# Optimization experiments

Measured on AMD Instinct MI355X. Metric: run time of the kernel, lower is better.

The kernel has to match this reference:

```python
import jax, jax.numpy as jnp
import numpy as np

NIBBLE_SHIFTS = jnp.arange(8, dtype=jnp.int32) * 4


def _unpack_int4(packed):
    # packed: [..., P] int32 -> [..., P*8] int32 values in [0, 15]
    vals = (packed[..., None] >> NIBBLE_SHIFTS) & 0xF
    return vals.reshape(*packed.shape[:-1], packed.shape[-1] * 8)


def setup_inputs() -> dict:
    key = jax.random.key(0)
    k1, k2, k3, k4, k5, k6 = jax.random.split(key, 6)
    M, K, N, G = 4096, 4096, 11008, 128
    inp = jax.random.normal(k1, (M, K), dtype=jnp.float32)
    qweight = jax.random.randint(k2, (K, N // 8), 0, 2147483647, dtype=jnp.int32)
    woq_scales = jax.random.uniform(k3, (K // G, N), dtype=jnp.float32)
    woq_qzeros = jax.random.randint(k4, (K // G, N // 8), 0, 2147483647, dtype=jnp.int32)
    woq_bias = jax.random.normal(k5, (N,), dtype=jnp.float32)
    mul = jax.random.normal(k6, (M, N), dtype=jnp.float32)
    return {"inp": inp, "qweight": qweight, "woq_scales": woq_scales,
            "woq_qzeros": woq_qzeros, "woq_bias": woq_bias, "mul": mul,
            "group_size": G}


def reference(inp, qweight, woq_scales, woq_qzeros, woq_bias, mul, group_size):
    K = qweight.shape[0]
    # dequantize int4 weights: w = (q - z) * scale, per group of `group_size` K-rows
    w_int = _unpack_int4(qweight).astype(jnp.float32)            # [K, N]
    z_int = _unpack_int4(woq_qzeros).astype(jnp.float32)         # [K/G, N]
    zeros_full = jnp.repeat(z_int, group_size, axis=0)           # [K, N]
    scales_full = jnp.repeat(woq_scales, group_size, axis=0)     # [K, N]
    w = (w_int - zeros_full) * scales_full                       # [K, N]
    woq_out = inp @ w + woq_bias                                 # [M, N]
    return jax.nn.silu(woq_out) * mul
```

## Files before the change

kernel.cpp:

```cpp
#include <hip/hip_runtime.h>
#include <hip/hip_bf16.h>

typedef __attribute__((ext_vector_type(8))) short short8;
typedef __attribute__((ext_vector_type(4))) short short4v;
typedef __attribute__((ext_vector_type(4))) float float4v;

__device__ __forceinline__ short f2bf(float f) {
  union { float f; unsigned u; } v; v.f = f;
  unsigned r = v.u + 0x7fffu + ((v.u >> 16) & 1u);
  return (short)(r >> 16);
}

typedef const __attribute__((address_space(1))) unsigned int* as1_u32p;
typedef __attribute__((address_space(3))) unsigned int* as3_u32p;

__device__ __forceinline__ void gl_lds16(const void* g, void* l) {
  __builtin_amdgcn_global_load_lds((as1_u32p)g, (as3_u32p)l, 16, 0, 0);
}

__global__ __launch_bounds__(256, 4)
void dequant_kernel(const int* __restrict__ qw,
                    const float* __restrict__ scales,
                    const int* __restrict__ qzeros,
                    short* __restrict__ Bt,
                    int K, int N, int G)
{
  constexpr int KP = 72;
  __shared__ short Ls[256 * KP];
  const int N8  = N >> 3;
  const int k0  = blockIdx.x * 64;
  const int n0  = blockIdx.y * 256;
  const int n80 = blockIdx.y * 32;
  const int g   = k0 / G;
  const int t   = threadIdx.x;
  const int kloc = t >> 3;
  const int w4   = (t & 7) * 4;

  const int4 z4 = *(const int4*)(qzeros + (size_t)g * N8 + n80 + w4);
  const int za[4] = {z4.x, z4.y, z4.z, z4.w};
  float sc[32];
  #pragma unroll
  for (int ii = 0; ii < 8; ++ii)
    *(float4v*)(sc + ii * 4) =
        *(const float4v*)(scales + (size_t)g * N + n0 + w4 * 8 + ii * 4);

  #pragma unroll
  for (int kh = 0; kh < 2; ++kh) {
    const int k = kloc + kh * 32;
    const int4 q4 = *(const int4*)(qw + (size_t)(k0 + k) * N8 + n80 + w4);
    const int qa[4] = {q4.x, q4.y, q4.z, q4.w};
    #pragma unroll
    for (int ii = 0; ii < 4; ++ii) {
      #pragma unroll
      for (int j = 0; j < 8; ++j) {
        const float z = (float)((za[ii] >> (4 * j)) & 0xF);
        const float q = (float)((qa[ii] >> (4 * j)) & 0xF);
        Ls[(w4 * 8 + ii * 8 + j) * KP + k] = f2bf((q - z) * sc[ii * 8 + j]);
      }
    }
  }
  __syncthreads();

  #pragma unroll
  for (int it = 0; it < 8; ++it) {
    const int idx = t + it * 256;
    const int row = idx >> 3;
    const int ch  = (idx & 7) * 8;
    const short8 v = *(const short8*)(&Ls[row * KP + ch]);
    *(short8*)(Bt + (size_t)(n0 + row) * K + k0 + ch) = v;
  }
}

__global__ __launch_bounds__(256, 2)
void dequant_kernel_v0(const int* __restrict__ qw,
                       const float* __restrict__ scales,
                       const int* __restrict__ qzeros,
                       short* __restrict__ Bt,
                       int K, int N, int G)
{
  __shared__ short Ls[128 * 64];
  const int N8  = N >> 3;
  const int k0  = blockIdx.x * 64;
  const int n80 = blockIdx.y * 16;
  const int g   = k0 / G;
  const int tid  = threadIdx.x;
  const int lane = tid & 63;
  const int w    = tid >> 6;

  const int4 q4 = *(const int4*)(qw + (size_t)(k0 + lane) * N8 + n80 + w * 4);
  const int4 z4 = *(const int4*)(qzeros + (size_t)g * N8 + n80 + w * 4);
  const int qa[4] = {q4.x, q4.y, q4.z, q4.w};
  const int za[4] = {z4.x, z4.y, z4.z, z4.w};

  #pragma unroll
  for (int it = 0; it < 4; ++it) {
    const int n8l = w * 4 + it;
    const float4v s0 = *(const float4v*)(scales + (size_t)g * N + (n80 + n8l) * 8);
    const float4v s1 = *(const float4v*)(scales + (size_t)g * N + (n80 + n8l) * 8 + 4);
    const float sc[8] = {s0[0], s0[1], s0[2], s0[3], s1[0], s1[1], s1[2], s1[3]};
    const int wq = qa[it], wz = za[it];
    #pragma unroll
    for (int j = 0; j < 8; ++j) {
      const float z = (float)((wz >> (4 * j)) & 0xF);
      const float q = (float)((wq >> (4 * j)) & 0xF);
      Ls[(n8l * 8 + j) * 64 + lane] = f2bf((q - z) * sc[j]);
    }
  }
  __syncthreads();

  #pragma unroll
  for (int it = 0; it < 4; ++it) {
    const int c   = tid + it * 256;
    const int row = c >> 3;
    const int off = (c & 7) * 8;
    const short8 v = *(const short8*)(&Ls[row * 64 + off]);
    *(short8*)(Bt + (size_t)(n80 * 8 + row) * K + k0 + off) = v;
  }
}

__global__ __launch_bounds__(256, 4)
void aconv_kernel(const float* __restrict__ in, short* __restrict__ out, long long n)
{
  const long long i = ((long long)blockIdx.x * blockDim.x + threadIdx.x) * 8;
  if (i >= n) return;
  const float4v a = *(const float4v*)(in + i);
  const float4v b = *(const float4v*)(in + i + 4);
  short8 h;
  h[0] = f2bf(a[0]); h[1] = f2bf(a[1]); h[2] = f2bf(a[2]); h[3] = f2bf(a[3]);
  h[4] = f2bf(b[0]); h[5] = f2bf(b[1]); h[6] = f2bf(b[2]); h[7] = f2bf(b[3]);
  *(short8*)(out + i) = h;
}

__global__ __launch_bounds__(512, 2)
void gemm256_silu_mul_kernel(const short* __restrict__ A,
                             const short* __restrict__ Bt,
                             const float* __restrict__ bias,
                             const float* __restrict__ mulp,
                             float*       __restrict__ out,
                             int M, int N, int K)
{
  __shared__ short L[2][2][16384];

  const int tid  = threadIdx.x;
  const int lane = tid & 63;
  const int wave = tid >> 6;
  const int wm   = wave >> 2;
  const int wn   = wave & 3;

  const int nwg = gridDim.x;
  const int q8 = nwg >> 3, r8 = nwg & 7;
  const int xcd = blockIdx.x & 7, sub = blockIdx.x >> 3;
  const int swz = (xcd < r8 ? xcd * (q8 + 1) : r8 * (q8 + 1) + (xcd - r8) * q8) + sub;
  const int nbx = N >> 8;
  const int bx = swz % nbx, by = swz / nbx;
  const int m0 = by << 8, n0 = bx << 8;

  const short* Ab = A  + (size_t)m0 * K;
  const short* Bb = Bt + (size_t)n0 * K;

  const int srow = lane >> 2;
  const int scol = (((lane & 3) ^ ((lane & 32) >> 4))) * 8;
  const int fm = lane & 15;
  const int ko = ((lane >> 4) * 8) ^ ((fm & 8) ? 16 : 0);

  const int BG0 = wave * 2;
  const int BG1 = wave * 2 + 1;
  const int AEg = (wave & 3) + (wave >> 2) * 8;
  const int ALg = AEg + 4;

  float4v acc[8][4];
  #pragma unroll
  for (int i = 0; i < 8; ++i)
    #pragma unroll
    for (int j = 0; j < 4; ++j)
      acc[i][j] = (float4v){0.f, 0.f, 0.f, 0.f};

  const int NT = K >> 6;

  auto stage2 = [&](int buf, int ab, int g, const short* __restrict__ base, int kk) {
    #pragma unroll
    for (int ks = 0; ks < 2; ++ks)
      gl_lds16(base + (size_t)(g * 16 + srow) * K + kk + ks * 32 + scol,
               &L[buf][ab][(g * 2 + ks) * 512]);
  };

  stage2(0, 0, AEg, Ab, 0);
  stage2(0, 1, BG0, Bb, 0);
  stage2(0, 1, BG1, Bb, 0);
  stage2(0, 0, ALg, Ab, 0);
  asm volatile("s_waitcnt vmcnt(4)" ::: "memory");
  __builtin_amdgcn_s_barrier();

  for (int t = 0; t < NT; ++t) {
    const int cur = t & 1;
    const int nxt = cur ^ 1;
    const int kk1 = (t + 1) << 6;
    const bool pf = (t + 1) < NT;

    short8 af[4][2], bf[4][2];

    #pragma unroll
    for (int i = 0; i < 4; ++i)
      #pragma unroll
      for (int ks = 0; ks < 2; ++ks)
        af[i][ks] = *(const short8*)(
            &L[cur][0][((wm * 8 + i) * 2 + ks) * 512 + fm * 32 + ko]);
    #pragma unroll
    for (int j = 0; j < 4; j += 2)
      #pragma unroll
      for (int ks = 0; ks < 2; ++ks)
        bf[j][ks] = *(const short8*)(
            &L[cur][1][((wn * 4 + j) * 2 + ks) * 512 + fm * 32 + ko]);
    if (pf) stage2(nxt, 0, AEg, Ab, kk1);
    __builtin_amdgcn_s_barrier();
    asm volatile("s_waitcnt lgkmcnt(0)" ::: "memory");
    __builtin_amdgcn_sched_barrier(0);
    __builtin_amdgcn_s_setprio(1);
    #pragma unroll
    for (int i = 0; i < 4; ++i)
      #pragma unroll
      for (int j = 0; j < 4; j += 2)
        #pragma unroll
        for (int ks = 0; ks < 2; ++ks)
          acc[i][j] = __builtin_amdgcn_mfma_f32_16x16x32_bf16(
              af[i][ks], bf[j][ks], acc[i][j], 0, 0, 0);
    __builtin_amdgcn_s_setprio(0);
    if (pf) { asm volatile("s_waitcnt vmcnt(4)" ::: "memory"); }
    else    { asm volatile("s_waitcnt vmcnt(2)" ::: "memory"); }
    __builtin_amdgcn_s_barrier();

    #pragma unroll
    for (int j = 1; j < 4; j += 2)
      #pragma unroll
      for (int ks = 0; ks < 2; ++ks)
        bf[j][ks] = *(const short8*)(
            &L[cur][1][((wn * 4 + j) * 2 + ks) * 512 + fm * 32 + ko]);
    if (pf) stage2(nxt, 1, BG0, Bb, kk1);
    __builtin_amdgcn_s_barrier();
    asm volatile("s_waitcnt lgkmcnt(0)" ::: "memory");
    __builtin_amdgcn_sched_barrier(0);
    __builtin_amdgcn_s_setprio(1);
    #pragma unroll
    for (int i = 0; i < 4; ++i)
      #pragma unroll
      for (int j = 1; j < 4; j += 2)
        #pragma unroll
        for (int ks = 0; ks < 2; ++ks)
          acc[i][j] = __builtin_amdgcn_mfma_f32_16x16x32_bf16(
              af[i][ks], bf[j][ks], acc[i][j], 0, 0, 0);
    __builtin_amdgcn_s_setprio(0);
    if (pf) { asm volatile("s_waitcnt vmcnt(4)" ::: "memory"); }
    else    { asm volatile("s_waitcnt vmcnt(0)" ::: "memory"); }
    __builtin_amdgcn_s_barrier();

    #pragma unroll
    for (int i = 0; i < 4; ++i)
      #pragma unroll
      for (int ks = 0; ks < 2; ++ks)
        af[i][ks] = *(const short8*)(
            &L[cur][0][((wm * 8 + 4 + i) * 2 + ks) * 512 + fm * 32 + ko]);
    if (pf) stage2(nxt, 1, BG1, Bb, kk1);
    __builtin_amdgcn_s_barrier();
    asm volatile("s_waitcnt lgkmcnt(0)" ::: "memory");
    __builtin_amdgcn_sched_barrier(0);
    __builtin_amdgcn_s_setprio(1);
    #pragma unroll
    for (int i = 0; i < 4; ++i)
      #pragma unroll
      for (int j = 0; j < 4; j += 2)
        #pragma unroll
        for (int ks = 0; ks < 2; ++ks)
          acc[4 + i][j] = __builtin_amdgcn_mfma_f32_16x16x32_bf16(
              af[i][ks], bf[j][ks], acc[4 + i][j], 0, 0, 0);
    __builtin_amdgcn_s_setprio(0);
    __builtin_amdgcn_s_barrier();

    if (pf) stage2(nxt, 0, ALg, Ab, kk1);
    __builtin_amdgcn_s_barrier();
    __builtin_amdgcn_s_setprio(1);
    #pragma unroll
    for (int i = 0; i < 4; ++i)
      #pragma unroll
      for (int j = 1; j < 4; j += 2)
        #pragma unroll
        for (int ks = 0; ks < 2; ++ks)
          acc[4 + i][j] = __builtin_amdgcn_mfma_f32_16x16x32_bf16(
              af[i][ks], bf[j][ks], acc[4 + i][j], 0, 0, 0);
    __builtin_amdgcn_s_setprio(0);
    if (pf) { asm volatile("s_waitcnt vmcnt(4)" ::: "memory"); }
    __builtin_amdgcn_s_barrier();
  }

  const int cn  = lane & 15;
  const int cr4 = (lane >> 4) * 4;
  #pragma unroll
  for (int mt = 0; mt < 8; ++mt) {
    #pragma unroll
    for (int nt = 0; nt < 4; ++nt) {
      const int n  = n0 + wn * 64 + nt * 16 + cn;
      const float bn = bias[n];
      #pragma unroll
      for (int i = 0; i < 4; ++i) {
        const int m = m0 + wm * 128 + mt * 16 + cr4 + i;
        float x = acc[mt][nt][i] + bn;
        float s = x / (1.0f + __expf(-x));
        out[(size_t)m * N + n] = s * mulp[(size_t)m * N + n];
      }
    }
  }
}

__global__ __launch_bounds__(256, 2)
void gemm_silu_mul_kernel(const short* __restrict__ A,
                          const short* __restrict__ Bt,
                          const float* __restrict__ bias,
                          const float* __restrict__ mulp,
                          float*       __restrict__ out,
                          int M, int N, int K)
{
  __shared__ short As[128 * 64];
  __shared__ short Bs[128 * 64];

  const int tid  = threadIdx.x;
  const int lane = tid & 63;
  const int wave = tid >> 6;
  const int wr = (wave >> 1) * 64;
  const int wc = (wave & 1) * 64;
  const int m0 = blockIdx.y * 128;
  const int n0 = blockIdx.x * 128;

  float4v acc[4][4];
  #pragma unroll
  for (int i = 0; i < 4; ++i)
    #pragma unroll
    for (int j = 0; j < 4; ++j)
      acc[i][j] = (float4v){0.f, 0.f, 0.f, 0.f};

  const int fm = lane & 15;
  const int fk = (lane >> 4) * 8;
  const int srow = lane >> 3;
  const int scol = (lane & 7) * 8;

  for (int k0 = 0; k0 < K; k0 += 64) {
    #pragma unroll
    for (int c = 0; c < 4; ++c) {
      const int chunk = wave * 4 + c;
      const int row   = chunk * 8 + srow;
      gl_lds16(A  + (size_t)(m0 + row) * K + k0 + scol, &As[chunk * 512]);
      gl_lds16(Bt + (size_t)(n0 + row) * K + k0 + scol, &Bs[chunk * 512]);
    }
    __syncthreads();

    #pragma unroll
    for (int ks = 0; ks < 64; ks += 32) {
      short8 a[4], b[4];
      #pragma unroll
      for (int mt = 0; mt < 4; ++mt)
        a[mt] = *(const short8*)(&As[(wr + mt * 16 + fm) * 64 + ks + fk]);
      #pragma unroll
      for (int nt = 0; nt < 4; ++nt)
        b[nt] = *(const short8*)(&Bs[(wc + nt * 16 + fm) * 64 + ks + fk]);
      #pragma unroll
      for (int mt = 0; mt < 4; ++mt)
        #pragma unroll
        for (int nt = 0; nt < 4; ++nt)
          acc[mt][nt] = __builtin_amdgcn_mfma_f32_16x16x32_bf16(a[mt], b[nt], acc[mt][nt], 0, 0, 0);
    }
    __syncthreads();
  }

  const int cn = lane & 15;
  const int cr = (lane >> 4) * 4;
  #pragma unroll
  for (int mt = 0; mt < 4; ++mt) {
    #pragma unroll
    for (int nt = 0; nt < 4; ++nt) {
      const int n  = n0 + wc + nt * 16 + cn;
      const float bn = bias[n];
      #pragma unroll
      for (int i = 0; i < 4; ++i) {
        const int m = m0 + wr + mt * 16 + cr + i;
        float x = acc[mt][nt][i] + bn;
        float s = x / (1.0f + __expf(-x));
        out[(size_t)m * N + n] = s * mulp[(size_t)m * N + n];
      }
    }
  }
}

#define BM 128
#define BN 128
#define BK 64
#define LDA 72
#define LDB 72

__global__ __launch_bounds__(256, 2)
void woq_silu_mul_kernel(const float* __restrict__ inp, const int* __restrict__ qw,
                         const float* __restrict__ scales, const int* __restrict__ qzeros,
                         const float* __restrict__ bias, const float* __restrict__ mulp,
                         float* __restrict__ out, int M, int N, int K, int G)
{
  __shared__ short As[BM * LDA];
  __shared__ short Bs[BN * LDB];
  const int tid  = threadIdx.x;
  const int lane = tid & 63;
  const int wave = tid >> 6;
  const int wr = (wave >> 1) * 64;
  const int wc = (wave & 1) * 64;
  const int m0 = blockIdx.y * BM;
  const int n0 = blockIdx.x * BN;
  const int N8 = N >> 3;
  float4v acc[4][4];
  #pragma unroll
  for (int i = 0; i < 4; ++i)
    #pragma unroll
    for (int j = 0; j < 4; ++j)
      acc[i][j] = (float4v){0.f, 0.f, 0.f, 0.f};
  const int n8l  = tid >> 4;
  const int kloc = (tid & 15) * 4;
  const int fm = lane & 15;
  const int fk = (lane >> 4) * 8;
  for (int k0 = 0; k0 < K; k0 += BK) {
    #pragma unroll
    for (int i = 0; i < 8; ++i) {
      int f = tid + i * 256;
      int row = f >> 4;
      int col = (f & 15) * 4;
      float4v a4 = *(const float4v*)(inp + (size_t)(m0 + row) * K + k0 + col);
      short4v h;
      h[0] = f2bf(a4[0]); h[1] = f2bf(a4[1]); h[2] = f2bf(a4[2]); h[3] = f2bf(a4[3]);
      *(short4v*)(&As[row * LDA + col]) = h;
    }
    {
      const int g = k0 / G;
      const int n8g = (n0 >> 3) + n8l;
      const int zw = qzeros[(size_t)g * N8 + n8g];
      const float4v s0 = *(const float4v*)(scales + (size_t)g * N + n0 + n8l * 8);
      const float4v s1 = *(const float4v*)(scales + (size_t)g * N + n0 + n8l * 8 + 4);
      float sc[8] = {s0[0], s0[1], s0[2], s0[3], s1[0], s1[1], s1[2], s1[3]};
      int w[4];
      #pragma unroll
      for (int kk = 0; kk < 4; ++kk)
        w[kk] = qw[(size_t)(k0 + kloc + kk) * N8 + n8g];
      #pragma unroll
      for (int j = 0; j < 8; ++j) {
        const float zj = (float)((zw >> (4 * j)) & 0xF);
        const float sj = sc[j];
        short4v h;
        #pragma unroll
        for (int kk = 0; kk < 4; ++kk) {
          int q = (w[kk] >> (4 * j)) & 0xF;
          h[kk] = f2bf(((float)q - zj) * sj);
        }
        *(short4v*)(&Bs[(n8l * 8 + j) * LDB + kloc]) = h;
      }
    }
    __syncthreads();
    #pragma unroll
    for (int ks = 0; ks < BK; ks += 32) {
      short8 a[4], b[4];
      #pragma unroll
      for (int mt = 0; mt < 4; ++mt)
        a[mt] = *(const short8*)(&As[(wr + mt * 16 + fm) * LDA + ks + fk]);
      #pragma unroll
      for (int nt = 0; nt < 4; ++nt)
        b[nt] = *(const short8*)(&Bs[(wc + nt * 16 + fm) * LDB + ks + fk]);
      #pragma unroll
      for (int mt = 0; mt < 4; ++mt)
        #pragma unroll
        for (int nt = 0; nt < 4; ++nt)
          acc[mt][nt] = __builtin_amdgcn_mfma_f32_16x16x32_bf16(a[mt], b[nt], acc[mt][nt], 0, 0, 0);
    }
    __syncthreads();
  }
  const int cn = lane & 15;
  const int cr = (lane >> 4) * 4;
  #pragma unroll
  for (int mt = 0; mt < 4; ++mt) {
    #pragma unroll
    for (int nt = 0; nt < 4; ++nt) {
      const int n = n0 + wc + nt * 16 + cn;
      const float bn = bias[n];
      #pragma unroll
      for (int i = 0; i < 4; ++i) {
        const int m = m0 + wr + mt * 16 + cr + i;
        float x = acc[mt][nt][i] + bn;
        float s = x / (1.0f + __expf(-x));
        out[(size_t)m * N + n] = s * mulp[(size_t)m * N + n];
      }
    }
  }
}

extern "C" void kernel_launch(void* const* d_in, const int* in_sizes, int n_in,
                              void* d_out, int out_size, void* d_ws, size_t ws_size,
                              hipStream_t stream) {
  const float* inp    = (const float*)d_in[0];
  const int*   qw     = (const int*)d_in[1];
  const float* scales = (const float*)d_in[2];
  const int*   qzeros = (const int*)d_in[3];
  const float* bias   = (const float*)d_in[4];
  const float* mulp   = (const float*)d_in[5];
  float*       out    = (float*)d_out;

  const int N = in_sizes[4];
  const int K = (int)(((long long)in_sizes[1] * 8) / N);
  const int M = (int)((long long)in_sizes[0] / K);
  const int G = K / (in_sizes[2] / N);

  const size_t btBytes = (size_t)N * K * sizeof(short);
  const size_t aBytes  = (size_t)M * K * sizeof(short);

  if (ws_size >= btBytes + aBytes) {
    short* Bt  = (short*)d_ws;
    short* Abf = (short*)((char*)d_ws + btBytes);

    if ((N & 255) == 0 && (K & 63) == 0 && (64 % (K / (in_sizes[2] / N) > 64 ? 64 : 1)) == 0) {
      dim3 dq_grid(K / 64, N / 256);
      dequant_kernel<<<dq_grid, dim3(256), 0, stream>>>(qw, scales, qzeros, Bt, K, N, G);
    } else {
      dim3 dq_grid(K / 64, (N / 8) / 16);
      dequant_kernel_v0<<<dq_grid, dim3(256), 0, stream>>>(qw, scales, qzeros, Bt, K, N, G);
    }

    const long long nA = (long long)M * K;
    aconv_kernel<<<dim3((unsigned)((nA / 8 + 255) / 256)), dim3(256), 0, stream>>>(inp, Abf, nA);

    if ((M & 255) == 0 && (N & 255) == 0 && (K & 63) == 0) {
      dim3 grid((unsigned)((N >> 8) * (M >> 8)));
      gemm256_silu_mul_kernel<<<grid, dim3(512), 0, stream>>>(Abf, Bt, bias, mulp, out, M, N, K);
    } else {
      dim3 grid(N / 128, M / 128);
      gemm_silu_mul_kernel<<<grid, dim3(256), 0, stream>>>(Abf, Bt, bias, mulp, out, M, N, K);
    }
  } else {
    dim3 grid(N / BN, M / BM);
    woq_silu_mul_kernel<<<grid, dim3(256), 0, stream>>>(inp, qw, scales, qzeros,
                                                        bias, mulp, out, M, N, K, G);
  }
}
```

Measured before the change: 707.5 us.

## Fuse dequant and A-conversion launches; deepen GEMM prefetch to two stages ahead

The weight dequantization and the fp32-to-bf16 activation conversion now run in one launch, with the block index choosing which role a block takes, so one kernel launch and its tail are removed. Separately, the GEMM main loop now issues global-to-LDS loads two k-tiles ahead instead of one, with new vmcnt wait counts, so more memory latency can overlap MFMA work. The deeper prefetch relies on hand-tuned waitcnt values and on a reordered staging sequence that writes into the buffer currently being read. That raises the risk of LDS races and adds more outstanding loads per wave.

```diff
diff --git a/kernel.cpp b/kernel.cpp
--- a/kernel.cpp
+++ b/kernel.cpp
@@ -19,18 +19,36 @@
 }
 
 __global__ __launch_bounds__(256, 4)
-void dequant_kernel(const int* __restrict__ qw,
-                    const float* __restrict__ scales,
-                    const int* __restrict__ qzeros,
-                    short* __restrict__ Bt,
-                    int K, int N, int G)
+void prep_kernel(const int* __restrict__ qw,
+                 const float* __restrict__ scales,
+                 const int* __restrict__ qzeros,
+                 short* __restrict__ Bt,
+                 const float* __restrict__ inp,
+                 short* __restrict__ Abf,
+                 int K, int N, int G, int nDq, long long nA)
 {
   constexpr int KP = 72;
   __shared__ short Ls[256 * KP];
+
+  if ((int)blockIdx.x >= nDq) {
+    const long long i =
+        (((long long)blockIdx.x - nDq) * blockDim.x + threadIdx.x) * 8;
+    if (i >= nA) return;
+    const float4v a = *(const float4v*)(inp + i);
+    const float4v b = *(const float4v*)(inp + i + 4);
+    short8 h;
+    h[0] = f2bf(a[0]); h[1] = f2bf(a[1]); h[2] = f2bf(a[2]); h[3] = f2bf(a[3]);
+    h[4] = f2bf(b[0]); h[5] = f2bf(b[1]); h[6] = f2bf(b[2]); h[7] = f2bf(b[3]);
+    *(short8*)(Abf + i) = h;
+    return;
+  }
+
+  const int KB  = K >> 6;
   const int N8  = N >> 3;
-  const int k0  = blockIdx.x * 64;
-  const int n0  = blockIdx.y * 256;
-  const int n80 = blockIdx.y * 32;
+  const int k0  = ((int)blockIdx.x % KB) * 64;
+  const int nb  = (int)blockIdx.x / KB;
+  const int n0  = nb * 256;
+  const int n80 = nb * 32;
   const int g   = k0 / G;
   const int t   = threadIdx.x;
   const int kloc = t >> 3;
@@ -188,14 +206,23 @@
   stage2(0, 1, BG0, Bb, 0);
   stage2(0, 1, BG1, Bb, 0);
   stage2(0, 0, ALg, Ab, 0);
-  asm volatile("s_waitcnt vmcnt(4)" ::: "memory");
+  if (NT > 1) {
+    stage2(1, 0, AEg, Ab, 64);
+    stage2(1, 1, BG0, Bb, 64);
+    stage2(1, 1, BG1, Bb, 64);
+    asm volatile("s_waitcnt vmcnt(10)" ::: "memory");
+  } else {
+    asm volatile("s_waitcnt vmcnt(4)" ::: "memory");
+  }
   __builtin_amdgcn_s_barrier();
 
   for (int t = 0; t < NT; ++t) {
     const int cur = t & 1;
     const int nxt = cur ^ 1;
+    const bool i1 = (t + 1) < NT;
+    const bool i2 = (t + 2) < NT;
     const int kk1 = (t + 1) << 6;
-    const bool pf = (t + 1) < NT;
+    const int kk2 = (t + 2) << 6;
 
     short8 af[4][2], bf[4][2];
 
@@ -211,7 +238,7 @@
       for (int ks = 0; ks < 2; ++ks)
         bf[j][ks] = *(const short8*)(
             &L[cur][1][((wn * 4 + j) * 2 + ks) * 512 + fm * 32 + ko]);
-    if (pf) stage2(nxt, 0, AEg, Ab, kk1);
+    if (i1) stage2(nxt, 0, ALg, Ab, kk1);
     __builtin_amdgcn_s_barrier();
     asm volatile("s_waitcnt lgkmcnt(0)" ::: "memory");
     __builtin_amdgcn_sched_barrier(0);
@@ -225,8 +252,8 @@
           acc[i][j] = __builtin_amdgcn_mfma_f32_16x16x32_bf16(
               af[i][ks], bf[j][ks], acc[i][j], 0, 0, 0);
     __builtin_amdgcn_s_setprio(0);
-    if (pf) { asm volatile("s_waitcnt vmcnt(4)" ::: "memory"); }
-    else    { asm volatile("s_waitcnt vmcnt(2)" ::: "memory"); }
+    if (i1) { asm volatile("s_waitcnt vmcnt(10)" ::: "memory"); }
+    else    { asm volatile("s_waitcnt vmcnt(2)"  ::: "memory"); }
     __builtin_amdgcn_s_barrier();
 
     #pragma unroll
@@ -235,7 +262,7 @@
       for (int ks = 0; ks < 2; ++ks)
         bf[j][ks] = *(const short8*)(
             &L[cur][1][((wn * 4 + j) * 2 + ks) * 512 + fm * 32 + ko]);
-    if (pf) stage2(nxt, 1, BG0, Bb, kk1);
+    if (i2) stage2(cur, 0, AEg, Ab, kk2);
     __builtin_amdgcn_s_barrier();
     asm volatile("s_waitcnt lgkmcnt(0)" ::: "memory");
     __builtin_amdgcn_sched_barrier(0);
@@ -249,8 +276,9 @@
           acc[i][j] = __builtin_amdgcn_mfma_f32_16x16x32_bf16(
               af[i][ks], bf[j][ks], acc[i][j], 0, 0, 0);
     __builtin_amdgcn_s_setprio(0);
-    if (pf) { asm volatile("s_waitcnt vmcnt(4)" ::: "memory"); }
-    else    { asm volatile("s_waitcnt vmcnt(0)" ::: "memory"); }
+    if (i2)      { asm volatile("s_waitcnt vmcnt(10)" ::: "memory"); }
+    else if (i1) { asm volatile("s_waitcnt vmcnt(8)"  ::: "memory"); }
+    else         { asm volatile("s_waitcnt vmcnt(0)"  ::: "memory"); }
     __builtin_amdgcn_s_barrier();
 
     #pragma unroll
@@ -259,7 +287,7 @@
       for (int ks = 0; ks < 2; ++ks)
         af[i][ks] = *(const short8*)(
             &L[cur][0][((wm * 8 + 4 + i) * 2 + ks) * 512 + fm * 32 + ko]);
-    if (pf) stage2(nxt, 1, BG1, Bb, kk1);
+    if (i2) stage2(cur, 1, BG0, Bb, kk2);
     __builtin_amdgcn_s_barrier();
     asm volatile("s_waitcnt lgkmcnt(0)" ::: "memory");
     __builtin_amdgcn_sched_barrier(0);
@@ -275,7 +303,7 @@
     __builtin_amdgcn_s_setprio(0);
     __builtin_amdgcn_s_barrier();
 
-    if (pf) stage2(nxt, 0, ALg, Ab, kk1);
+    if (i2) stage2(cur, 1, BG1, Bb, kk2);
     __builtin_amdgcn_s_barrier();
     __builtin_amdgcn_s_setprio(1);
     #pragma unroll
@@ -287,7 +315,8 @@
           acc[4 + i][j] = __builtin_amdgcn_mfma_f32_16x16x32_bf16(
               af[i][ks], bf[j][ks], acc[4 + i][j], 0, 0, 0);
     __builtin_amdgcn_s_setprio(0);
-    if (pf) { asm volatile("s_waitcnt vmcnt(4)" ::: "memory"); }
+    if (i2)      { asm volatile("s_waitcnt vmcnt(10)" ::: "memory"); }
+    else if (i1) { asm volatile("s_waitcnt vmcnt(4)"  ::: "memory"); }
     __builtin_amdgcn_s_barrier();
   }
 
@@ -514,17 +543,20 @@
   if (ws_size >= btBytes + aBytes) {
     short* Bt  = (short*)d_ws;
     short* Abf = (short*)((char*)d_ws + btBytes);
-
-    if ((N & 255) == 0 && (K & 63) == 0 && (64 % (K / (in_sizes[2] / N) > 64 ? 64 : 1)) == 0) {
-      dim3 dq_grid(K / 64, N / 256);
-      dequant_kernel<<<dq_grid, dim3(256), 0, stream>>>(qw, scales, qzeros, Bt, K, N, G);
+    const long long nA = (long long)M * K;
+
+    const bool dqOk = (N & 255) == 0 && (K & 63) == 0 && G >= 64 && (G & 63) == 0
+                      && (nA & 7) == 0;
+    if (dqOk) {
+      const int nDq = (K / 64) * (N / 256);
+      const int nAc = (int)((nA / 8 + 255) / 256);
+      prep_kernel<<<dim3((unsigned)(nDq + nAc)), dim3(256), 0, stream>>>(
+          qw, scales, qzeros, Bt, inp, Abf, K, N, G, nDq, nA);
     } else {
       dim3 dq_grid(K / 64, (N / 8) / 16);
       dequant_kernel_v0<<<dq_grid, dim3(256), 0, stream>>>(qw, scales, qzeros, Bt, K, N, G);
-    }
-
-    const long long nA = (long long)M * K;
-    aconv_kernel<<<dim3((unsigned)((nA / 8 + 255) / 256)), dim3(256), 0, stream>>>(inp, Abf, nA);
+      aconv_kernel<<<dim3((unsigned)((nA / 8 + 255) / 256)), dim3(256), 0, stream>>>(inp, Abf, nA);
+    }
 
     if ((M & 255) == 0 && (N & 255) == 0 && (K & 63) == 0) {
       dim3 grid((unsigned)((N >> 8) * (M >> 8)));
```

Result: no change. 699.9 us (-1.1%).
